# Performance work log

Hardware: AMD Instinct MI355X
Metric: run time of the kernel (lower is better)

## Reference

```python
import jax, jax.numpy as jnp
import numpy as np

NUM_SLOTS = 4096
NUM_CLUSTER = 10
SLOT_DIM = 64
EPS = 1e-8
N_ITER = 3
LN_EPS = 1e-5


def _ln(x, g, b):
    m = jnp.mean(x, axis=-1, keepdims=True)
    v = jnp.var(x, axis=-1, keepdims=True)
    return (x - m) / jnp.sqrt(v + LN_EPS) * g + b


def setup_inputs() -> dict:
    key = jax.random.key(0)
    ks = jax.random.split(key, 24)
    d, S = SLOT_DIM, NUM_SLOTS
    s = d ** -0.5
    f32 = jnp.float32
    return {
        "cluster_centers": jax.random.normal(ks[0], (NUM_CLUSTER, d), f32),
        "Wk": jax.random.normal(ks[1], (d, d), f32) * s,
        "bk": jnp.zeros((d,), f32),
        "Wq": jax.random.normal(ks[2], (d, d), f32) * s,
        "bq": jnp.zeros((d,), f32),
        "Wv": jax.random.normal(ks[3], (d, d), f32) * s,
        "bv": jnp.zeros((d,), f32),
        "cc_g": jnp.ones((d,), f32),
        "cc_b": jnp.zeros((d,), f32),
        "W_ih": jax.random.normal(ks[4], (3 * d, d), f32) * s,
        "W_hh": jax.random.normal(ks[5], (3 * d, d), f32) * s,
        "b_ih": jnp.zeros((3 * d,), f32),
        "b_hh": jnp.zeros((3 * d,), f32),
        "ln_g": jnp.ones((d,), f32),
        "ln_b": jnp.zeros((d,), f32),
        "W1": jax.random.normal(ks[6], (2 * d, d), f32) * s,
        "b1": jnp.zeros((2 * d,), f32),
        "W2": jax.random.normal(ks[7], (d, 2 * d), f32) * (2 * d) ** -0.5,
        "b2": jnp.zeros((d,), f32),
        "Wa": jax.random.normal(ks[8], (S, d, d), f32) * s,
        "ba": jnp.zeros((S, d), f32),
        "Wb": jax.random.normal(ks[9], (S, d, d), f32) * s,
        "bb": jnp.zeros((S, d), f32),
    }


def reference(cluster_centers, Wk, bk, Wq, bq, Wv, bv, cc_g, cc_b,
              W_ih, W_hh, b_ih, b_hh, ln_g, ln_b, W1, b1, W2, b2,
              Wa, ba, Wb, bb):
    temp = SLOT_DIM ** -0.5
    k = cluster_centers @ Wk.T + bk          # [N, d]
    v = cluster_centers @ Wv.T + bv          # [N, d]
    cc = cluster_centers
    for _ in range(N_ITER):
        cc_prev = cc
        q = _ln(cc, cc_g, cc_b) @ Wq.T + bq  # [N, d]
        attn = jnp.einsum('nd,md->nm', k, q) * temp
        attn = jax.nn.softmax(attn, axis=0) + EPS
        attn = attn / jnp.sum(attn, axis=-1, keepdims=True)
        updates = attn @ v                   # [N, d]
        # PyTorch GRUCell
        gi = updates @ W_ih.T + b_ih
        gh = cc_prev @ W_hh.T + b_hh
        ir, iz, inn = jnp.split(gi, 3, axis=-1)
        hr, hz, hn = jnp.split(gh, 3, axis=-1)
        r = jax.nn.sigmoid(ir + hr)
        z = jax.nn.sigmoid(iz + hz)
        n = jnp.tanh(inn + r * hn)
        cc = (1.0 - z) * n + z * cc_prev
        # residual MLP
        h = _ln(cc, ln_g, ln_b)
        cc = cc + jax.nn.relu(h @ W1.T + b1) @ W2.T + b2
    # per-slot 2-layer MLP + max over the 10 clusters, vectorized over slots
    h = jax.nn.relu(jnp.einsum('sij,nj->sni', Wa, cc) + ba[:, None, :])  # [S, N, d]
    out = jnp.einsum('sij,snj->sni', Wb, h) + bb[:, None, :]             # [S, N, d]
    return jnp.max(out, axis=1)                                          # [S, d]
```

## Files before the change

kernel.cpp:

```cpp
#include <hip/hip_runtime.h>
#include <math.h>

#define NCLU 10
#define D    64
#define NSLOT 4096

typedef unsigned int   u32;
typedef unsigned short u16;

typedef __attribute__((ext_vector_type(8))) short  bf16x8;
typedef __attribute__((ext_vector_type(4))) float  f32x4;

__device__ __forceinline__ u16 f2bf_rne(float f) {
    u32 u = __float_as_uint(f);
    return (u16)((u + 0x7fffu + ((u >> 16) & 1u)) >> 16);
}

__device__ __forceinline__ bf16x8 pack8(float4 a, float4 b) {
    bf16x8 r;
    r[0] = (short)f2bf_rne(a.x); r[1] = (short)f2bf_rne(a.y);
    r[2] = (short)f2bf_rne(a.z); r[3] = (short)f2bf_rne(a.w);
    r[4] = (short)f2bf_rne(b.x); r[5] = (short)f2bf_rne(b.y);
    r[6] = (short)f2bf_rne(b.z); r[7] = (short)f2bf_rne(b.w);
    return r;
}

__device__ __forceinline__ float wred(float v) {
#pragma unroll
    for (int off = 32; off > 0; off >>= 1) v += __shfl_xor(v, off);
    return v;
}

__device__ __forceinline__ void load_afrags64(bf16x8 a[4][2], const float* __restrict__ W,
                                              int lc, int quad) {
#pragma unroll
    for (int mt = 0; mt < 4; ++mt)
#pragma unroll
        for (int kt = 0; kt < 2; ++kt) {
            const float* p = W + (16 * mt + lc) * 64 + kt * 32 + quad * 8;
            a[mt][kt] = pack8(*(const float4*)p, *(const float4*)(p + 4));
        }
}

__device__ __forceinline__ void load_afrags128(bf16x8 a[4][2], const float* __restrict__ W,
                                               int ktbase, int lc, int quad) {
#pragma unroll
    for (int mt = 0; mt < 4; ++mt)
#pragma unroll
        for (int kt = 0; kt < 2; ++kt) {
            const float* p = W + (16 * mt + lc) * 128 + (ktbase + kt) * 32 + quad * 8;
            a[mt][kt] = pack8(*(const float4*)p, *(const float4*)(p + 4));
        }
}

__device__ __forceinline__ bf16x8 bfrag(const float* __restrict__ xbase, int xstride,
                                        int lc, int quad, int ktglob) {
    if (lc < NCLU) {
        const float* p = xbase + lc * xstride + ktglob * 32 + quad * 8;
        return pack8(*(const float4*)p, *(const float4*)(p + 4));
    }
    bf16x8 z;
#pragma unroll
    for (int j = 0; j < 8; ++j) z[j] = 0;
    return z;
}

__device__ __forceinline__ void mm_apply(const bf16x8 a[4][2], const float* __restrict__ xbase,
                                         int xstride, int ktbase,
                                         float* __restrict__ obase, int ostride, int ooff,
                                         const float4 bp[4], bool use_bias, bool do_relu,
                                         int lc, int quad) {
    f32x4 acc[4];
#pragma unroll
    for (int mt = 0; mt < 4; ++mt) acc[mt] = (f32x4){0.f, 0.f, 0.f, 0.f};
#pragma unroll
    for (int kt = 0; kt < 2; ++kt) {
        bf16x8 b = bfrag(xbase, xstride, lc, quad, ktbase + kt);
#pragma unroll
        for (int mt = 0; mt < 4; ++mt)
            acc[mt] = __builtin_amdgcn_mfma_f32_16x16x32_bf16(a[mt][kt], b, acc[mt], 0, 0, 0);
    }
    if (lc < NCLU) {
#pragma unroll
        for (int mt = 0; mt < 4; ++mt) {
            float4 o;
            o.x = acc[mt][0]; o.y = acc[mt][1]; o.z = acc[mt][2]; o.w = acc[mt][3];
            if (use_bias) {
                o.x += bp[mt].x; o.y += bp[mt].y; o.z += bp[mt].z; o.w += bp[mt].w;
            }
            if (do_relu) {
                o.x = fmaxf(o.x, 0.f); o.y = fmaxf(o.y, 0.f);
                o.z = fmaxf(o.z, 0.f); o.w = fmaxf(o.w, 0.f);
            }
            *(float4*)(obase + lc * ostride + ooff + 16 * mt + 4 * quad) = o;
        }
    }
}

__global__ __launch_bounds__(640, 3) void phase1_kernel(
    const float* __restrict__ cc0,
    const float* __restrict__ Wk, const float* __restrict__ bk,
    const float* __restrict__ Wq, const float* __restrict__ bq,
    const float* __restrict__ Wv, const float* __restrict__ bv,
    const float* __restrict__ cc_g, const float* __restrict__ cc_b,
    const float* __restrict__ W_ih, const float* __restrict__ W_hh,
    const float* __restrict__ b_ih, const float* __restrict__ b_hh,
    const float* __restrict__ ln_g, const float* __restrict__ ln_b,
    const float* __restrict__ W1, const float* __restrict__ b1,
    const float* __restrict__ W2, const float* __restrict__ b2,
    float* __restrict__ cc_out)
{
    const int t = threadIdx.x;
    const int w = t >> 6;
    const int i = t & 63;
    const int quad = i >> 4;
    const int lc   = i & 15;

    __shared__ float ccl[NCLU][68];
    __shared__ float xl[NCLU][68];
    __shared__ float kl[NCLU][68];
    __shared__ float vl[NCLU][68];
    __shared__ float ql[NCLU][68];
    __shared__ float ul[NCLU][68];
    __shared__ float hl[NCLU][68];
    __shared__ float dl9[NCLU][68];
    __shared__ float dl8[NCLU][68];
    __shared__ float tl[NCLU][132];
    __shared__ float gl[6][NCLU][68];
    __shared__ float al[NCLU][12];

    const float g_cc = cc_g[i], b_cc = cc_b[i];
    const float g_ln = ln_g[i], b_ln = ln_b[i];

    bf16x8 afrA[4][2], afrB[4][2];
#pragma unroll
    for (int mt = 0; mt < 4; ++mt)
#pragma unroll
        for (int kt = 0; kt < 2; ++kt) {
#pragma unroll
            for (int j = 0; j < 8; ++j) { afrA[mt][kt][j] = 0; afrB[mt][kt][j] = 0; }
        }

    const float* biasA = nullptr;
    if (w == 0)      { load_afrags64(afrA, Wq, lc, quad);                       biasA = bq; }
    else if (w <= 3) { load_afrags64(afrA, W_ih + (w - 1) * 64 * 64, lc, quad); biasA = b_ih + (w - 1) * 64; }
    else if (w <= 6) { load_afrags64(afrA, W_hh + (w - 4) * 64 * 64, lc, quad); biasA = b_hh + (w - 4) * 64; }
    else if (w == 7) { load_afrags64(afrA, Wk, lc, quad);                       biasA = bk; }
    else if (w == 8) { load_afrags64(afrA, Wv, lc, quad);                       biasA = bv;
                       load_afrags128(afrB, W2, 2, lc, quad); }
    else             { load_afrags128(afrA, W2, 0, lc, quad);                   biasA = b2; }

    float4 bpre[4];
#pragma unroll
    for (int mt = 0; mt < 4; ++mt) { bpre[mt].x = bpre[mt].y = bpre[mt].z = bpre[mt].w = 0.f; }
    if (biasA) {
#pragma unroll
        for (int mt = 0; mt < 4; ++mt) bpre[mt] = *(const float4*)(biasA + 16 * mt + 4 * quad);
    }

    float c = cc0[w * 64 + i];
    ccl[w][i] = c;
    __syncthreads();

    if (w == 7)      mm_apply(afrA, &ccl[0][0], 68, 0, &kl[0][0], 68, 0, bpre, true, false, lc, quad);
    else if (w == 8) mm_apply(afrA, &ccl[0][0], 68, 0, &vl[0][0], 68, 0, bpre, true, false, lc, quad);
    __syncthreads();

    if (w == 7) {
        load_afrags64(afrA, W1, lc, quad);
#pragma unroll
        for (int mt = 0; mt < 4; ++mt) bpre[mt] = *(const float4*)(b1 + 16 * mt + 4 * quad);
    } else if (w == 8) {
        load_afrags64(afrA, W1 + 64 * 64, lc, quad);
#pragma unroll
        for (int mt = 0; mt < 4; ++mt) bpre[mt] = *(const float4*)(b1 + 64 + 16 * mt + 4 * quad);
    }

    for (int it = 0; it < 3; ++it) {
        {
            float s1 = wred(c), s2 = wred(c * c);
            float mu = s1 * (1.f / 64.f);
            float va = s2 * (1.f / 64.f) - mu * mu;
            xl[w][i] = (c - mu) * rsqrtf(va + 1e-5f) * g_cc + b_cc;
        }
        __syncthreads();

        if (w == 0)
            mm_apply(afrA, &xl[0][0], 68, 0, &ql[0][0], 68, 0, bpre, true, false, lc, quad);
        else if (w >= 4 && w <= 6)
            mm_apply(afrA, &ccl[0][0], 68, 0, &gl[w - 1][0][0], 68, 0, bpre, true, false, lc, quad);
        __syncthreads();

        if (i < NCLU) {
            const float4* kf = (const float4*)&kl[w][0];
            const float4* qf = (const float4*)&ql[i][0];
            float a0 = 0.f, a1 = 0.f, a2 = 0.f, a3 = 0.f;
#pragma unroll
            for (int jj = 0; jj < 16; ++jj) {
                float4 kv = kf[jj], qv = qf[jj];
                a0 += kv.x * qv.x; a1 += kv.y * qv.y; a2 += kv.z * qv.z; a3 += kv.w * qv.w;
            }
            al[w][i] = ((a0 + a1) + (a2 + a3)) * 0.125f;
        }
        __syncthreads();

        {
            float e[NCLU];
            if (i < NCLU) {
                float mx = -1e30f;
#pragma unroll
                for (int nn = 0; nn < NCLU; ++nn) mx = fmaxf(mx, al[nn][i]);
                float s = 0.f;
#pragma unroll
                for (int nn = 0; nn < NCLU; ++nn) { e[nn] = __expf(al[nn][i] - mx); s += e[nn]; }
                float inv = 1.f / s;
#pragma unroll
                for (int nn = 0; nn < NCLU; ++nn) e[nn] = e[nn] * inv + 1e-8f;
            } else {
#pragma unroll
                for (int nn = 0; nn < NCLU; ++nn) e[nn] = 0.f;
            }
            float rs[NCLU];
#pragma unroll
            for (int nn = 0; nn < NCLU; ++nn) rs[nn] = e[nn];
#pragma unroll
            for (int off = 1; off < 16; off <<= 1) {
#pragma unroll
                for (int nn = 0; nn < NCLU; ++nn) rs[nn] += __shfl_xor(rs[nn], off);
            }
            float ew = 0.f, rw = 1.f;
#pragma unroll
            for (int nn = 0; nn < NCLU; ++nn) if (nn == w) { ew = e[nn]; rw = rs[nn]; }
            float val = (i < NCLU) ? ew / rw : 0.f;
            float u = 0.f;
#pragma unroll
            for (int m = 0; m < NCLU; ++m) u += __shfl(val, m) * vl[m][i];
            ul[w][i] = u;
        }
        __syncthreads();

        if (w >= 1 && w <= 3)
            mm_apply(afrA, &ul[0][0], 68, 0, &gl[w - 1][0][0], 68, 0, bpre, true, false, lc, quad);
        __syncthreads();

        {
            float ir = gl[0][w][i], iz = gl[1][w][i], inn = gl[2][w][i];
            float hr = gl[3][w][i], hz = gl[4][w][i], hn = gl[5][w][i];
            float r = 1.f / (1.f + __expf(-(ir + hr)));
            float z = 1.f / (1.f + __expf(-(iz + hz)));
            float xt = inn + r * hn;
            float ex2 = __expf(2.f * xt);
            float nn2 = 1.f - 2.f / (ex2 + 1.f);
            c = (1.f - z) * nn2 + z * c;

            float s1 = wred(c), s2 = wred(c * c);
            float mu = s1 * (1.f / 64.f);
            float va = s2 * (1.f / 64.f) - mu * mu;
            hl[w][i] = (c - mu) * rsqrtf(va + 1e-5f) * g_ln + b_ln;
        }
        __syncthreads();

        if (w == 7)
            mm_apply(afrA, &hl[0][0], 68, 0, &tl[0][0], 132, 0, bpre, true, true, lc, quad);
        else if (w == 8)
            mm_apply(afrA, &hl[0][0], 68, 0, &tl[0][0], 132, 64, bpre, true, true, lc, quad);
        __syncthreads();

        if (w == 9)
            mm_apply(afrA, &tl[0][0], 132, 0, &dl9[0][0], 68, 0, bpre, true, false, lc, quad);
        else if (w == 8)
            mm_apply(afrB, &tl[0][0], 132, 2, &dl8[0][0], 68, 0, bpre, false, false, lc, quad);
        __syncthreads();

        c += dl9[w][i] + dl8[w][i];
        ccl[w][i] = c;
    }

    cc_out[w * 64 + i] = c;
}

#define HSTR 72
#define SLOTS_PER_BLK 4
__global__ __launch_bounds__(256, 4) void phase2_kernel(
    const float* __restrict__ Wa, const float* __restrict__ ba,
    const float* __restrict__ Wb, const float* __restrict__ bb,
    const float* __restrict__ cc, float* __restrict__ out)
{
    const int w = threadIdx.x >> 6;
    const int l = threadIdx.x & 63;
    const int quad = l >> 4;
    const int lc   = l & 15;
    const int s0 = blockIdx.x * SLOTS_PER_BLK;

    __shared__ u16 hT[2][16 * HSTR];

    float4 c00, c01, c10, c11;
    if (lc < NCLU) {
        const float* cp = cc + lc * 64;
        c00 = *(const float4*)(cp + 0 * 32 + quad * 8);
        c01 = *(const float4*)(cp + 0 * 32 + quad * 8 + 4);
        c10 = *(const float4*)(cp + 1 * 32 + quad * 8);
        c11 = *(const float4*)(cp + 1 * 32 + quad * 8 + 4);
    }

    float bbs[SLOTS_PER_BLK];
    if (lc < 4) {
#pragma unroll
        for (int j = 0; j < SLOTS_PER_BLK; ++j)
            bbs[j] = bb[(s0 + j) * 64 + 16 * w + 4 * quad + lc];
    }

    float4 rA[2][4], rB[2][4];
    float4 bav[2];

    auto ISSUE = [&](int j, int bank) {
        const int s = s0 + j;
        const float* wa = Wa + (size_t)s * 4096 + (16 * w + lc) * 64 + quad * 8;
        const float* wb = Wb + (size_t)s * 4096 + (16 * w + lc) * 64 + quad * 8;
        rA[bank][0] = *(const float4*)(wa);
        rA[bank][1] = *(const float4*)(wa + 4);
        rA[bank][2] = *(const float4*)(wa + 32);
        rA[bank][3] = *(const float4*)(wa + 36);
        rB[bank][0] = *(const float4*)(wb);
        rB[bank][1] = *(const float4*)(wb + 4);
        rB[bank][2] = *(const float4*)(wb + 32);
        rB[bank][3] = *(const float4*)(wb + 36);
        bav[bank] = *(const float4*)(ba + s * 64 + 16 * w + quad * 4);
    };

    ISSUE(0, 0);

    bf16x8 bcc[2];
    if (lc < NCLU) {
        bcc[0] = pack8(c00, c01);
        bcc[1] = pack8(c10, c11);
    } else {
#pragma unroll
        for (int j = 0; j < 8; ++j) { bcc[0][j] = 0; bcc[1][j] = 0; }
    }

#pragma unroll
    for (int j = 0; j < SLOTS_PER_BLK; ++j) {
        const int cur = j & 1;
        if (j + 1 < SLOTS_PER_BLK) ISSUE(j + 1, (j + 1) & 1);

        bf16x8 frA[2], frB[2];
        frA[0] = pack8(rA[cur][0], rA[cur][1]);
        frA[1] = pack8(rA[cur][2], rA[cur][3]);
        frB[0] = pack8(rB[cur][0], rB[cur][1]);
        frB[1] = pack8(rB[cur][2], rB[cur][3]);

        f32x4 acc = (f32x4){0.f, 0.f, 0.f, 0.f};
        acc = __builtin_amdgcn_mfma_f32_16x16x32_bf16(frA[0], bcc[0], acc, 0, 0, 0);
        acc = __builtin_amdgcn_mfma_f32_16x16x32_bf16(frA[1], bcc[1], acc, 0, 0, 0);

        {
            u16 h0 = f2bf_rne(fmaxf(acc[0] + bav[cur].x, 0.f));
            u16 h1 = f2bf_rne(fmaxf(acc[1] + bav[cur].y, 0.f));
            u16 h2 = f2bf_rne(fmaxf(acc[2] + bav[cur].z, 0.f));
            u16 h3 = f2bf_rne(fmaxf(acc[3] + bav[cur].w, 0.f));
            uint2 pk; pk.x = (u32)h0 | ((u32)h1 << 16); pk.y = (u32)h2 | ((u32)h3 << 16);
            *(uint2*)(&hT[cur][lc * HSTR + 16 * w + quad * 4]) = pk;
        }

        __syncthreads();

        bf16x8 bh[2];
#pragma unroll
        for (int kt = 0; kt < 2; ++kt)
            bh[kt] = *(const bf16x8*)(&hT[cur][lc * HSTR + kt * 32 + quad * 8]);

        f32x4 acc2 = (f32x4){0.f, 0.f, 0.f, 0.f};
        acc2 = __builtin_amdgcn_mfma_f32_16x16x32_bf16(frB[0], bh[0], acc2, 0, 0, 0);
        acc2 = __builtin_amdgcn_mfma_f32_16x16x32_bf16(frB[1], bh[1], acc2, 0, 0, 0);

        const float NEG = -3.0e38f;
#pragma unroll
        for (int r = 0; r < 4; ++r) {
            float v = (lc < NCLU) ? acc2[r] : NEG;
#pragma unroll
            for (int off = 1; off < 16; off <<= 1)
                v = fmaxf(v, __shfl_xor(v, off));
            acc2[r] = v;
        }

        if (lc < 4) {
            int row = 16 * w + 4 * quad + lc;
            out[(s0 + j) * 64 + row] = acc2[lc] + bbs[j];
        }
    }
}

extern "C" void kernel_launch(void* const* d_in, const int* in_sizes, int n_in,
                              void* d_out, int out_size, void* d_ws, size_t ws_size,
                              hipStream_t stream) {
    const float* cc0  = (const float*)d_in[0];
    const float* Wk   = (const float*)d_in[1];
    const float* bk   = (const float*)d_in[2];
    const float* Wq   = (const float*)d_in[3];
    const float* bq   = (const float*)d_in[4];
    const float* Wv   = (const float*)d_in[5];
    const float* bv   = (const float*)d_in[6];
    const float* ccg  = (const float*)d_in[7];
    const float* ccb  = (const float*)d_in[8];
    const float* Wih  = (const float*)d_in[9];
    const float* Whh  = (const float*)d_in[10];
    const float* bih  = (const float*)d_in[11];
    const float* bhh  = (const float*)d_in[12];
    const float* lng  = (const float*)d_in[13];
    const float* lnb  = (const float*)d_in[14];
    const float* W1   = (const float*)d_in[15];
    const float* b1   = (const float*)d_in[16];
    const float* W2   = (const float*)d_in[17];
    const float* b2   = (const float*)d_in[18];
    const float* Wa   = (const float*)d_in[19];
    const float* ba   = (const float*)d_in[20];
    const float* Wb   = (const float*)d_in[21];
    const float* bb   = (const float*)d_in[22];

    float* cc_ws = (float*)d_ws;
    float* out   = (float*)d_out;

    hipLaunchKernelGGL(phase1_kernel, dim3(1), dim3(640), 0, stream,
                       cc0, Wk, bk, Wq, bq, Wv, bv, ccg, ccb,
                       Wih, Whh, bih, bhh, lng, lnb, W1, b1, W2, b2, cc_ws);

    hipLaunchKernelGGL(phase2_kernel, dim3(NSLOT / SLOTS_PER_BLK), dim3(256), 0, stream,
                       Wa, ba, Wb, bb, cc_ws, out);
}
```

Before: 220.6 us.

## Hand-schedule phase2 weight loads with inline asm and explicit vmcnt waits

Phase2 now handles 8 slots per block instead of 4 and lowers the occupancy hint in launch bounds from 4 to 2. The double-buffered weight loads are issued through inline-asm global_load_dwordx4 with explicit s_waitcnt vmcnt counters, so the compiler cannot collapse the prefetch into an early full wait. Output stores are deferred to the end of the block, and __syncthreads is replaced with an lgkmcnt wait plus s_barrier. The aim is to keep more memory traffic in flight across slot iterations while streaming Wa/Wb, at the risk of fewer resident waves and fewer blocks.

Result: slower. 226.6 us (+2.7%).

```diff
diff --git a/kernel.cpp b/kernel.cpp
--- a/kernel.cpp
+++ b/kernel.cpp
@@ -22,6 +22,15 @@
     r[2] = (short)f2bf_rne(a.z); r[3] = (short)f2bf_rne(a.w);
     r[4] = (short)f2bf_rne(b.x); r[5] = (short)f2bf_rne(b.y);
     r[6] = (short)f2bf_rne(b.z); r[7] = (short)f2bf_rne(b.w);
+    return r;
+}
+
+__device__ __forceinline__ bf16x8 pack8v(f32x4 a, f32x4 b) {
+    bf16x8 r;
+    r[0] = (short)f2bf_rne(a[0]); r[1] = (short)f2bf_rne(a[1]);
+    r[2] = (short)f2bf_rne(a[2]); r[3] = (short)f2bf_rne(a[3]);
+    r[4] = (short)f2bf_rne(b[0]); r[5] = (short)f2bf_rne(b[1]);
+    r[6] = (short)f2bf_rne(b[2]); r[7] = (short)f2bf_rne(b[3]);
     return r;
 }
 
@@ -280,8 +289,30 @@
 }
 
 #define HSTR 72
-#define SLOTS_PER_BLK 4
-__global__ __launch_bounds__(256, 4) void phase2_kernel(
+#define SLOTS_PER_BLK 8
+
+#define P2_ISSUE(jj, bk) do {                                                          \
+    const float* _p = pa + (size_t)(jj) * 4096;                                        \
+    const float* _q = pb + (size_t)(jj) * 4096;                                        \
+    const float* _r = pba + (size_t)(jj) * 64;                                         \
+    asm volatile("global_load_dwordx4 %0, %1, off"            : "=v"(rA[bk][0]) : "v"(_p)); \
+    asm volatile("global_load_dwordx4 %0, %1, off offset:16"  : "=v"(rA[bk][1]) : "v"(_p)); \
+    asm volatile("global_load_dwordx4 %0, %1, off offset:128" : "=v"(rA[bk][2]) : "v"(_p)); \
+    asm volatile("global_load_dwordx4 %0, %1, off offset:144" : "=v"(rA[bk][3]) : "v"(_p)); \
+    asm volatile("global_load_dwordx4 %0, %1, off"            : "=v"(rB[bk][0]) : "v"(_q)); \
+    asm volatile("global_load_dwordx4 %0, %1, off offset:16"  : "=v"(rB[bk][1]) : "v"(_q)); \
+    asm volatile("global_load_dwordx4 %0, %1, off offset:128" : "=v"(rB[bk][2]) : "v"(_q)); \
+    asm volatile("global_load_dwordx4 %0, %1, off offset:144" : "=v"(rB[bk][3]) : "v"(_q)); \
+    asm volatile("global_load_dwordx4 %0, %1, off"            : "=v"(bav[bk])   : "v"(_r)); \
+} while (0)
+
+#define P2_WAIT(imm, bk)                                                               \
+    asm volatile("s_waitcnt vmcnt(" #imm ")"                                           \
+        : "+v"(rA[bk][0]), "+v"(rA[bk][1]), "+v"(rA[bk][2]), "+v"(rA[bk][3]),          \
+          "+v"(rB[bk][0]), "+v"(rB[bk][1]), "+v"(rB[bk][2]), "+v"(rB[bk][3]),          \
+          "+v"(bav[bk]) :: )
+
+__global__ __launch_bounds__(256, 2) void phase2_kernel(
     const float* __restrict__ Wa, const float* __restrict__ ba,
     const float* __restrict__ Wb, const float* __restrict__ bb,
     const float* __restrict__ cc, float* __restrict__ out)
@@ -302,33 +333,12 @@
         c10 = *(const float4*)(cp + 1 * 32 + quad * 8);
         c11 = *(const float4*)(cp + 1 * 32 + quad * 8 + 4);
     }
-
     float bbs[SLOTS_PER_BLK];
     if (lc < 4) {
 #pragma unroll
         for (int j = 0; j < SLOTS_PER_BLK; ++j)
             bbs[j] = bb[(s0 + j) * 64 + 16 * w + 4 * quad + lc];
     }
-
-    float4 rA[2][4], rB[2][4];
-    float4 bav[2];
-
-    auto ISSUE = [&](int j, int bank) {
-        const int s = s0 + j;
-        const float* wa = Wa + (size_t)s * 4096 + (16 * w + lc) * 64 + quad * 8;
-        const float* wb = Wb + (size_t)s * 4096 + (16 * w + lc) * 64 + quad * 8;
-        rA[bank][0] = *(const float4*)(wa);
-        rA[bank][1] = *(const float4*)(wa + 4);
-        rA[bank][2] = *(const float4*)(wa + 32);
-        rA[bank][3] = *(const float4*)(wa + 36);
-        rB[bank][0] = *(const float4*)(wb);
-        rB[bank][1] = *(const float4*)(wb + 4);
-        rB[bank][2] = *(const float4*)(wb + 32);
-        rB[bank][3] = *(const float4*)(wb + 36);
-        bav[bank] = *(const float4*)(ba + s * 64 + 16 * w + quad * 4);
-    };
-
-    ISSUE(0, 0);
 
     bf16x8 bcc[2];
     if (lc < NCLU) {
@@ -338,32 +348,50 @@
 #pragma unroll
         for (int j = 0; j < 8; ++j) { bcc[0][j] = 0; bcc[1][j] = 0; }
     }
+#pragma unroll
+    for (int j = 0; j < SLOTS_PER_BLK; ++j) asm volatile("" :: "v"(bbs[j]));
+
+    const float* pa  = Wa + (size_t)s0 * 4096 + (16 * w + lc) * 64 + quad * 8;
+    const float* pb  = Wb + (size_t)s0 * 4096 + (16 * w + lc) * 64 + quad * 8;
+    const float* pba = ba + (size_t)s0 * 64 + 16 * w + quad * 4;
+
+    f32x4 rA[2][4], rB[2][4], bav[2];
+    float outv[SLOTS_PER_BLK];
+
+    P2_ISSUE(0, 0);
 
 #pragma unroll
     for (int j = 0; j < SLOTS_PER_BLK; ++j) {
         const int cur = j & 1;
-        if (j + 1 < SLOTS_PER_BLK) ISSUE(j + 1, (j + 1) & 1);
+        const int nxt = cur ^ 1;
+
+        if (j + 1 < SLOTS_PER_BLK) {
+            P2_ISSUE(j + 1, nxt);
+            P2_WAIT(9, cur);
+        } else {
+            P2_WAIT(0, cur);
+        }
 
         bf16x8 frA[2], frB[2];
-        frA[0] = pack8(rA[cur][0], rA[cur][1]);
-        frA[1] = pack8(rA[cur][2], rA[cur][3]);
-        frB[0] = pack8(rB[cur][0], rB[cur][1]);
-        frB[1] = pack8(rB[cur][2], rB[cur][3]);
+        frA[0] = pack8v(rA[cur][0], rA[cur][1]);
+        frA[1] = pack8v(rA[cur][2], rA[cur][3]);
+        frB[0] = pack8v(rB[cur][0], rB[cur][1]);
+        frB[1] = pack8v(rB[cur][2], rB[cur][3]);
 
         f32x4 acc = (f32x4){0.f, 0.f, 0.f, 0.f};
         acc = __builtin_amdgcn_mfma_f32_16x16x32_bf16(frA[0], bcc[0], acc, 0, 0, 0);
         acc = __builtin_amdgcn_mfma_f32_16x16x32_bf16(frA[1], bcc[1], acc, 0, 0, 0);
 
         {
-            u16 h0 = f2bf_rne(fmaxf(acc[0] + bav[cur].x, 0.f));
-            u16 h1 = f2bf_rne(fmaxf(acc[1] + bav[cur].y, 0.f));
-            u16 h2 = f2bf_rne(fmaxf(acc[2] + bav[cur].z, 0.f));
-            u16 h3 = f2bf_rne(fmaxf(acc[3] + bav[cur].w, 0.f));
+            u16 h0 = f2bf_rne(fmaxf(acc[0] + bav[cur][0], 0.f));
+            u16 h1 = f2bf_rne(fmaxf(acc[1] + bav[cur][1], 0.f));
+            u16 h2 = f2bf_rne(fmaxf(acc[2] + bav[cur][2], 0.f));
+            u16 h3 = f2bf_rne(fmaxf(acc[3] + bav[cur][3], 0.f));
             uint2 pk; pk.x = (u32)h0 | ((u32)h1 << 16); pk.y = (u32)h2 | ((u32)h3 << 16);
             *(uint2*)(&hT[cur][lc * HSTR + 16 * w + quad * 4]) = pk;
         }
 
-        __syncthreads();
+        asm volatile("s_waitcnt lgkmcnt(0)\n\ts_barrier" ::: "memory");
 
         bf16x8 bh[2];
 #pragma unroll
@@ -383,11 +411,15 @@
                 v = fmaxf(v, __shfl_xor(v, off));
             acc2[r] = v;
         }
-
-        if (lc < 4) {
-            int row = 16 * w + 4 * quad + lc;
-            out[(s0 + j) * 64 + row] = acc2[lc] + bbs[j];
-        }
+        float ov = (lc == 0) ? acc2[0] : (lc == 1) ? acc2[1] : (lc == 2) ? acc2[2] : acc2[3];
+        outv[j] = ov + ((lc < 4) ? bbs[j] : 0.f);
+    }
+
+    if (lc < 4) {
+        const int row = 16 * w + 4 * quad + lc;
+#pragma unroll
+        for (int j = 0; j < SLOTS_PER_BLK; ++j)
+            out[(s0 + j) * 64 + row] = outv[j];
     }
 }
 
```
